# Kernel tuning notes

Hardware: AMD Instinct MI355X
Metric: run time of the kernel (lower is better)

The kernel has to match this reference:

```python
import jax, jax.numpy as jnp
import numpy as np

WD, WH, WW = 7, 7, 7  # 3D window size


def _relative_position_index():
    # Matches the torch buffer construction exactly.
    coords = np.stack(np.meshgrid(np.arange(WD), np.arange(WH), np.arange(WW), indexing='ij'))  # [3,wd,wh,ww]
    cf = coords.reshape(3, -1)                      # [3, n]
    rel = cf[:, :, None] - cf[:, None, :]           # [3, n, n]
    rel = rel.transpose(1, 2, 0).copy()             # [n, n, 3]
    rel[..., 0] += WD - 1
    rel[..., 1] += WH - 1
    rel[..., 2] += WW - 1
    rel[..., 0] *= (2 * WH - 1) * (2 * WW - 1)
    rel[..., 1] *= (2 * WW - 1)
    return rel.sum(-1).astype(np.int32)             # [n, n] in [0, 2197)


def setup_inputs() -> dict:
    key = jax.random.key(0)
    ks = jax.random.split(key, 10)
    DIM, H = 192, 6
    B, N, NW = 256, WD * WH * WW, 64  # b = batch*num_windows, NW divides B
    TABLE = (2 * WD - 1) * (2 * WH - 1) * (2 * WW - 1)  # 2197
    w_std = 0.02
    mask = jnp.where(jax.random.uniform(ks[2], (NW, N, N)) < 0.1, -100.0, 0.0).astype(jnp.float32)
    return {
        'x_q': jax.random.normal(ks[0], (B, N, DIM), jnp.float32),
        'x_kv': jax.random.normal(ks[1], (B, N, DIM), jnp.float32),
        'mask': mask,
        'q_w': jax.random.normal(ks[3], (DIM, DIM), jnp.float32) * w_std,
        'q_b': jnp.zeros((DIM,), jnp.float32),
        'kv_w': jax.random.normal(ks[4], (2 * DIM, DIM), jnp.float32) * w_std,
        'kv_b': jnp.zeros((2 * DIM,), jnp.float32),
        'proj_w': jax.random.normal(ks[5], (DIM, DIM), jnp.float32) * w_std,
        'proj_b': jnp.zeros((DIM,), jnp.float32),
        'rpb_table': jax.random.normal(ks[6], (TABLE, H), jnp.float32) * w_std,
        'rpi': jnp.asarray(_relative_position_index()),
    }


def reference(x_q, x_kv, mask, q_w, q_b, kv_w, kv_b, proj_w, proj_b, rpb_table, rpi):
    b, n, c = x_q.shape
    h = rpb_table.shape[-1]
    d = c // h
    scale = d ** (-0.5)
    # projections (torch Linear: y = x @ W.T + b)
    q = (x_q @ q_w.T + q_b).reshape(b, n, h, d)
    kv = x_kv @ kv_w.T + kv_b                      # [b, n, 2c]
    k = kv[..., :c].reshape(b, n, h, d)
    v = kv[..., c:].reshape(b, n, h, d)
    # windowed QK^T
    attn = jnp.einsum('bnhd,bmhd->bhnm', q * scale, k)  # [b, h, n, n]
    # gathered relative-position bias
    rpb = rpb_table[rpi[:n, :n].reshape(-1)].reshape(n, n, h).transpose(2, 0, 1)  # [h, n, n]
    attn = attn + rpb[None]
    # window mask add
    nw = mask.shape[0]
    attn = attn.reshape(b // nw, nw, h, n, n) + mask[None, :, None]
    attn = jax.nn.softmax(attn.reshape(b, h, n, n), axis=-1)
    out = jnp.einsum('bhnm,bmhd->bnhd', attn, v).reshape(b, n, c)
    return out @ proj_w.T + proj_b
```

## Files before the change

### kernel.cpp

```cpp
#include <hip/hip_runtime.h>
#include <hip/hip_bf16.h>
#include <cstdint>

#define B_    256
#define N_    343
#define C_    192
#define H_    6
#define D_    32
#define NW_   64
#define M_    (B_*N_)
#define NN_   (N_*N_)
#define VTS_  352
#define VLS_  360
#define RPG_  86
#define SCALE_ 0.17677669529663687f
#define LOG2E_ 1.4426950408889634f
#define SCALE_LOG2E_ (SCALE_ * LOG2E_)

typedef unsigned short ushort_t;
typedef __attribute__((ext_vector_type(8))) short short8;
typedef __attribute__((ext_vector_type(4))) float f32x4;
typedef __attribute__((ext_vector_type(16))) float f32x16;

__device__ __forceinline__ float b2f(unsigned int u) {
    return __uint_as_float(u << 16);
}
__device__ __forceinline__ unsigned int f2b(float f) {
    unsigned int x = __float_as_uint(f);
    x += 0x7FFFu + ((x >> 16) & 1u);
    return x >> 16;
}
__device__ __forceinline__ unsigned int cvt_pk(float a, float b) {
    unsigned int r;
    asm("v_cvt_pk_bf16_f32 %0, %1, %2" : "=v"(r) : "v"(a), "v"(b));
    return r;
}
__device__ __forceinline__ void pswap(unsigned int &x, unsigned int &y) {
    asm("v_permlane32_swap_b32 %0, %1" : "+v"(x), "+v"(y));
}

__global__ __launch_bounds__(256) void wcvt(
    const float* __restrict__ qw, const float* __restrict__ kvw,
    const float* __restrict__ pw, ushort_t* __restrict__ wb)
{
    int i = blockIdx.x * 256 + threadIdx.x;
    if (i >= 36864) return;
    float4 v;
    if (i < 9216)       v = ((const float4*)qw)[i];
    else if (i < 27648) v = ((const float4*)kvw)[i - 9216];
    else                v = ((const float4*)pw)[i - 27648];
    uint2 u;
    u.x = cvt_pk(v.x, v.y);
    u.y = cvt_pk(v.z, v.w);
    ((uint2*)wb)[i] = u;
}

__global__ __launch_bounds__(512, 2) void gemm_qkv(
    const float* __restrict__ xq, const float* __restrict__ xkv,
    const ushort_t* __restrict__ wb,
    const float* __restrict__ qbias, const float* __restrict__ kvbias,
    ushort_t* __restrict__ qx, ushort_t* __restrict__ kx,
    ushort_t* __restrict__ vtb)
{
    __shared__ ushort_t wls[192 * 200];
    __shared__ float    bls[192];

    const int t = threadIdx.x, wv = t >> 6, lane = t & 63;
    const int quad = lane >> 4, col = lane & 15;
    const int lbid = (blockIdx.x & 7) * 64 + (blockIdx.x >> 3);
    const int start = lbid * 2 + (lbid < 5 ? lbid : 5);
    const int cnt = 2 + (lbid < 5 ? 1 : 0);

    for (int ji = 0; ji < cnt; ++ji) {
        const int job = start + ji;
        const int mgrp = job / 3, jsel = job - mgrp * 3;
        const int m0 = mgrp * 256;
        const float* Xf = (jsel == 0) ? xq : xkv;
        const float* bias = (jsel == 0) ? qbias : (jsel == 1 ? kvbias : kvbias + 192);
        const float alpha = (jsel == 0) ? SCALE_LOG2E_ : 1.0f;

        if (ji) __syncthreads();
        {
            const ushort_t* W = wb + (size_t)jsel * 36864;
            for (int c = t; c < 4608; c += 512) {
                int row = c / 24, off = (c % 24) * 8;
                *(short8*)(wls + row * 200 + off) = *(const short8*)(W + row * 192 + off);
            }
            if (t < 48) ((float4*)bls)[t] = ((const float4*)bias)[t];
        }

        short8 xf[2][6];
        #pragma unroll
        for (int sub = 0; sub < 2; ++sub) {
            const float* xp = Xf + (size_t)(m0 + wv * 32 + sub * 16 + col) * 192;
            float4 a0[6], a1[6];
            #pragma unroll
            for (int kt = 0; kt < 6; ++kt) {
                a0[kt] = *(const float4*)(xp + kt * 32 + quad * 8);
                a1[kt] = *(const float4*)(xp + kt * 32 + quad * 8 + 4);
            }
            #pragma unroll
            for (int kt = 0; kt < 6; ++kt) {
                union { short8 s; unsigned int u[4]; } f;
                f.u[0] = cvt_pk(a0[kt].x, a0[kt].y);
                f.u[1] = cvt_pk(a0[kt].z, a0[kt].w);
                f.u[2] = cvt_pk(a1[kt].x, a1[kt].y);
                f.u[3] = cvt_pk(a1[kt].z, a1[kt].w);
                xf[sub][kt] = f.s;
            }
        }
        __syncthreads();

        f32x4 acc[2][12] = {};
        #pragma unroll
        for (int kt = 0; kt < 6; ++kt)
            #pragma unroll
            for (int ct = 0; ct < 12; ++ct) {
                short8 wf = *(const short8*)(wls + (ct * 16 + col) * 200 + kt * 32 + quad * 8);
                acc[0][ct] = __builtin_amdgcn_mfma_f32_16x16x32_bf16(wf, xf[0][kt], acc[0][ct], 0, 0, 0);
                acc[1][ct] = __builtin_amdgcn_mfma_f32_16x16x32_bf16(wf, xf[1][kt], acc[1][ct], 0, 0, 0);
            }

        if (jsel < 2) {
            ushort_t* o16 = (jsel == 0) ? qx : kx;
            #pragma unroll
            for (int sub = 0; sub < 2; ++sub) {
                int m = m0 + wv * 32 + sub * 16 + col;
                int bb = m / N_, nn = m - bb * N_;
                #pragma unroll
                for (int ct = 0; ct < 12; ++ct) {
                    float4 bv = *(const float4*)(bls + ct * 16 + quad * 4);
                    int hh = ct >> 1;
                    int dbase = (ct & 1) * 16 + quad * 4;
                    float v0 = (acc[sub][ct][0] + bv.x) * alpha;
                    float v1 = (acc[sub][ct][1] + bv.y) * alpha;
                    float v2 = (acc[sub][ct][2] + bv.z) * alpha;
                    float v3 = (acc[sub][ct][3] + bv.w) * alpha;
                    uint2 pk;
                    pk.x = cvt_pk(v0, v1);
                    pk.y = cvt_pk(v2, v3);
                    *(uint2*)(o16 + (((size_t)bb * H_ + hh) * N_ + nn) * D_ + dbase) = pk;
                }
            }
        } else {
            #pragma unroll
            for (int sub = 0; sub < 2; ++sub) {
                int m = m0 + wv * 32 + sub * 16 + col;
                int bb = m / N_, nn = m - bb * N_;
                #pragma unroll
                for (int ct = 0; ct < 12; ++ct) {
                    float4 bv = *(const float4*)(bls + ct * 16 + quad * 4);
                    int hh = ct >> 1;
                    int d0 = (ct & 1) * 16 + quad * 4;
                    unsigned int u01 = cvt_pk(acc[sub][ct][0] + bv.x, acc[sub][ct][1] + bv.y);
                    unsigned int u23 = cvt_pk(acc[sub][ct][2] + bv.z, acc[sub][ct][3] + bv.w);
                    ushort_t* vp = vtb + (((size_t)bb * H_ + hh) * D_ + d0) * VTS_ + nn;
                    vp[0]            = (ushort_t)u01;
                    vp[VTS_]         = (ushort_t)(u01 >> 16);
                    vp[2 * VTS_]     = (ushort_t)u23;
                    vp[3 * VTS_]     = (ushort_t)(u23 >> 16);
                }
            }
        }
    }
}

__global__ __launch_bounds__(512, 2) void gemm_out(
    const ushort_t* __restrict__ aob, const ushort_t* __restrict__ wb,
    const float* __restrict__ pbias, float* __restrict__ out)
{
    __shared__ ushort_t wls[192 * 200];

    const int t = threadIdx.x, wv = t >> 6, lane = t & 63;
    const int quad = lane >> 4, col = lane & 15;
    const int m0 = blockIdx.x * 256;
    const ushort_t* W = wb + (size_t)3 * 36864;

    short8 xf[2][6];
    #pragma unroll
    for (int sub = 0; sub < 2; ++sub) {
        const ushort_t* xp = aob + (size_t)(m0 + wv * 32 + sub * 16 + col) * 192;
        #pragma unroll
        for (int kt = 0; kt < 6; ++kt)
            xf[sub][kt] = *(const short8*)(xp + kt * 32 + quad * 8);
    }
    for (int c = t; c < 4608; c += 512) {
        int row = c / 24, off = (c % 24) * 8;
        *(short8*)(wls + row * 200 + off) = *(const short8*)(W + row * 192 + off);
    }
    __syncthreads();

    f32x4 acc[2][12] = {};
    #pragma unroll
    for (int kt = 0; kt < 6; ++kt)
        #pragma unroll
        for (int ct = 0; ct < 12; ++ct) {
            short8 wf = *(const short8*)(wls + (ct * 16 + col) * 200 + kt * 32 + quad * 8);
            acc[0][ct] = __builtin_amdgcn_mfma_f32_16x16x32_bf16(wf, xf[0][kt], acc[0][ct], 0, 0, 0);
            acc[1][ct] = __builtin_amdgcn_mfma_f32_16x16x32_bf16(wf, xf[1][kt], acc[1][ct], 0, 0, 0);
        }

    #pragma unroll
    for (int sub = 0; sub < 2; ++sub) {
        int m = m0 + wv * 32 + sub * 16 + col;
        #pragma unroll
        for (int ct = 0; ct < 12; ++ct) {
            float4 bv = *(const float4*)(pbias + ct * 16 + quad * 4);
            float4 vo;
            vo.x = acc[sub][ct][0] + bv.x; vo.y = acc[sub][ct][1] + bv.y;
            vo.z = acc[sub][ct][2] + bv.z; vo.w = acc[sub][ct][3] + bv.w;
            *(float4*)(out + (size_t)m * 192 + ct * 16 + quad * 4) = vo;
        }
    }
}

__global__ __launch_bounds__(256) void rpb_gather_b(
    const float* __restrict__ table, const int* __restrict__ rpi,
    ushort_t* __restrict__ rpbt)
{
    int n = blockIdx.x;
    for (int m = threadIdx.x; m < N_; m += 256) {
        int id = rpi[n * N_ + m];
        int mg = m >> 2, mi = m & 3;
        #pragma unroll
        for (int h = 0; h < H_; ++h)
            rpbt[((((size_t)h * RPG_ + mg) * N_) + n) * 4 + mi] =
                (ushort_t)f2b(table[(size_t)id * H_ + h] * LOG2E_);
    }
}

__global__ __launch_bounds__(256) void mask_bits(
    const float* __restrict__ mask, unsigned int* __restrict__ mbt)
{
    int gw   = blockIdx.x * 4 + (threadIdx.x >> 6);
    int lane = threadIdx.x & 63;
    int n = gw % N_, w = gw / N_;
    if (w >= NW_) return;
    const float* mrow = mask + ((size_t)w * N_ + n) * N_;
    #pragma unroll
    for (int seg = 0; seg < 6; ++seg) {
        int m = seg * 64 + lane;
        float v = (m < N_) ? mrow[m] : -100.f;
        unsigned long long bm = __ballot(v > -50.f);
        if (lane < 2)
            mbt[((size_t)w * 12 + seg * 2 + lane) * N_ + n] =
                (unsigned int)(bm >> (lane * 32));
    }
}

__global__ __launch_bounds__(256) void vt_pad(ushort_t* __restrict__ vtb)
{
    int bh = blockIdx.x;
    for (int i = threadIdx.x; i < D_ * (VTS_ - N_); i += 256) {
        int d = i / (VTS_ - N_), m = N_ + i % (VTS_ - N_);
        vtb[((size_t)bh * D_ + d) * VTS_ + m] = 0;
    }
}

__global__ __launch_bounds__(256, 3) void attn_mfma(
    const ushort_t* __restrict__ qb, const ushort_t* __restrict__ kb,
    const ushort_t* __restrict__ vtb, const ushort_t* __restrict__ rpbt,
    const unsigned int* __restrict__ mbt, ushort_t* __restrict__ aob)
{
    __shared__ ushort_t ks[352 * 40];
    __shared__ ushort_t vls[32 * VLS_];

    const int t = threadIdx.x, wv = t >> 6, lane = t & 63;
    const int hh = lane >> 5, c = lane & 31;
    const int lid = blockIdx.x;
    const int wg = (lid & 7) * 576 + (lid >> 3);
    const int qt = wg % 3;
    const int bhx = wg / 3;
    const int h = bhx % H_, b = bhx / H_;
    const int bh = b * H_ + h;
    const int w  = b & (NW_ - 1);
    const int n0 = qt * 128 + wv * 32;

    const ushort_t* kbase = kb + (size_t)bh * (N_ * D_);
    for (int cc = t; cc < (N_ * D_) / 8; cc += 256) {
        int row = cc >> 2, off = (cc & 3) * 8;
        *(short8*)(ks + row * 40 + off) = *(const short8*)(kbase + cc * 8);
    }
    for (int cc = t; cc < 360; cc += 256) ks[13720 + cc] = 0;

    {
        const int vd = t >> 3, vj0 = t & 7;
        const ushort_t* vsrc = vtb + (size_t)bh * (D_ * VTS_) + (size_t)vd * VTS_;
        ushort_t* vdst = vls + vd * VLS_;
        #pragma unroll
        for (int j = 0; j < 6; ++j) {
            int jj = vj0 + j * 8;
            if (jj < 44)
                *(short8*)(vdst + jj * 8) = *(const short8*)(vsrc + jj * 8);
        }
    }

    int nn = n0 + c; if (nn > N_ - 1) nn = N_ - 1;
    const ushort_t* qp = qb + ((size_t)bh * N_ + nn) * D_;
    short8 qf0 = *(const short8*)(qp + hh * 8);
    short8 qf1 = *(const short8*)(qp + 16 + hh * 8);

    unsigned int dwv[12];
    {
        const unsigned int* mbp = mbt + (size_t)w * 12 * N_ + nn;
        #pragma unroll
        for (int i = 0; i < 12; ++i) dwv[i] = mbp[i * N_];
    }
    const uint2* rp2h = (const uint2*)rpbt + (size_t)h * (RPG_ * N_) + nn
                        + (size_t)hh * N_;

    __syncthreads();

    f32x16 oacc = {};
    float sum = 0.f;

    #pragma unroll
    for (int kt = 0; kt < 11; ++kt) {
        const ushort_t* krow = ks + (kt * 32 + c) * 40 + hh * 8;
        short8 ka  = *(const short8*)(krow);
        short8 kb2 = *(const short8*)(krow + 16);
        unsigned int nibs = dwv[kt] >> (hh * 4);
        f32x16 s;
        #pragma unroll
        for (int g = 0; g < 4; ++g) {
            if (kt == 10 && g == 3) {
                s[12] = -3.0e38f; s[13] = -3.0e38f;
                s[14] = -3.0e38f; s[15] = -3.0e38f;
            } else {
                uint2 rv = rp2h[(kt * 8 + 2 * g) * (size_t)N_];
                unsigned int nib = (nibs >> (g * 8)) & 0xFu;
                s[4*g+0] = (nib & 1u) ? b2f(rv.x & 0xffffu) : -3.0e38f;
                s[4*g+1] = (nib & 2u) ? b2f(rv.x >> 16)     : -3.0e38f;
                s[4*g+2] = (nib & 4u) ? b2f(rv.y & 0xffffu) : -3.0e38f;
                s[4*g+3] = (nib & 8u) ? b2f(rv.y >> 16)     : -3.0e38f;
            }
        }
        s = __builtin_amdgcn_mfma_f32_32x32x16_bf16(ka,  qf0, s, 0, 0, 0);
        s = __builtin_amdgcn_mfma_f32_32x32x16_bf16(kb2, qf1, s, 0, 0, 0);

        unsigned int pk[8];
        #pragma unroll
        for (int g = 0; g < 4; ++g) {
            float e0 = __builtin_exp2f(s[4*g+0]);
            float e1 = __builtin_exp2f(s[4*g+1]);
            float e2 = __builtin_exp2f(s[4*g+2]);
            float e3 = __builtin_exp2f(s[4*g+3]);
            sum += (e0 + e1) + (e2 + e3);
            pk[2*g]   = cvt_pk(e0, e1);
            pk[2*g+1] = cvt_pk(e2, e3);
        }
        pswap(pk[0], pk[2]);
        pswap(pk[1], pk[3]);
        pswap(pk[4], pk[6]);
        pswap(pk[5], pk[7]);
        union { short8 s8; unsigned int u[4]; } pf1, pf2;
        pf1.u[0] = pk[0]; pf1.u[1] = pk[1]; pf1.u[2] = pk[2]; pf1.u[3] = pk[3];
        pf2.u[0] = pk[4]; pf2.u[1] = pk[5]; pf2.u[2] = pk[6]; pf2.u[3] = pk[7];

        const ushort_t* vrow = vls + c * VLS_ + kt * 32 + hh * 8;
        short8 vf1 = *(const short8*)(vrow);
        short8 vf2 = *(const short8*)(vrow + 16);
        oacc = __builtin_amdgcn_mfma_f32_32x32x16_bf16(vf1, pf1.s8, oacc, 0, 0, 0);
        oacc = __builtin_amdgcn_mfma_f32_32x32x16_bf16(vf2, pf2.s8, oacc, 0, 0, 0);
    }

    sum += __shfl_xor(sum, 32);

    int n = n0 + c;
    if (n < N_) {
        float inv = 1.0f / sum;
        ushort_t* op = aob + ((size_t)b * N_ + n) * C_ + h * D_ + hh * 4;
        #pragma unroll
        for (int g = 0; g < 4; ++g) {
            uint2 pkk;
            pkk.x = cvt_pk(oacc[4*g+0] * inv, oacc[4*g+1] * inv);
            pkk.y = cvt_pk(oacc[4*g+2] * inv, oacc[4*g+3] * inv);
            *(uint2*)(op + g * 8) = pkk;
        }
    }
}

extern "C" void kernel_launch(void* const* d_in, const int* in_sizes, int n_in,
                              void* d_out, int out_size, void* d_ws, size_t ws_size,
                              hipStream_t stream)
{
    const float* x_q    = (const float*)d_in[0];
    const float* x_kv   = (const float*)d_in[1];
    const float* mask   = (const float*)d_in[2];
    const float* q_w    = (const float*)d_in[3];
    const float* q_b    = (const float*)d_in[4];
    const float* kv_w   = (const float*)d_in[5];
    const float* kv_b   = (const float*)d_in[6];
    const float* proj_w = (const float*)d_in[7];
    const float* proj_b = (const float*)d_in[8];
    const float* rpb_t  = (const float*)d_in[9];
    const int*   rpi    = (const int*)d_in[10];
    float* out = (float*)d_out;

    const size_t QKV  = (size_t)B_ * H_ * N_ * D_;
    const size_t QKV2 = (size_t)B_ * H_ * D_ * VTS_;
    char* ws = (char*)d_ws;
    ushort_t* qx   = (ushort_t*)ws;
    ushort_t* kx   = qx + QKV;
    ushort_t* vtb  = kx + QKV;
    ushort_t* aob  = vtb + QKV2;
    ushort_t* rpbt = aob + QKV;
    ushort_t* wb   = rpbt + (size_t)H_ * RPG_ * N_ * 4;
    unsigned int* mbt = (unsigned int*)(wb + 147456);

    wcvt<<<144, 256, 0, stream>>>(q_w, kv_w, proj_w, wb);
    rpb_gather_b<<<N_, 256, 0, stream>>>(rpb_t, rpi, rpbt);
    mask_bits<<<(NW_ * N_) / 4, 256, 0, stream>>>(mask, mbt);
    vt_pad<<<B_ * H_, 256, 0, stream>>>(vtb);
    gemm_qkv<<<512, 512, 0, stream>>>(
        x_q, x_kv, wb, q_b, kv_b, qx, kx, vtb);
    attn_mfma<<<4608, 256, 0, stream>>>(qx, kx, vtb, rpbt, mbt, aob);
    gemm_out<<<343, 512, 0, stream>>>(aob, wb, proj_b, out);
}
```

Before: 389.7 us.

## Use atomic work queue in QKV GEMM and read K directly from global in attention

The QKV projection kernel drops its static job partition and pulls jobs from a global atomic counter, which wcvt resets. The counter lives at the start of the attention-output buffer, which is only written later. The attention kernel stops staging K in shared memory and loads K fragments straight from global memory. It also raises the occupancy hint from 3 to 7 blocks per CU, trading shared-memory reuse of K for more resident waves. The risks are extra global/L2 traffic for K and register pressure under the tighter launch bound.

```diff
diff --git a/kernel.cpp b/kernel.cpp
--- a/kernel.cpp
+++ b/kernel.cpp
@@ -13,6 +13,7 @@
 #define VTS_  352
 #define VLS_  360
 #define RPG_  86
+#define NJOB_ 1029
 #define SCALE_ 0.17677669529663687f
 #define LOG2E_ 1.4426950408889634f
 #define SCALE_LOG2E_ (SCALE_ * LOG2E_)
@@ -41,9 +42,11 @@
 
 __global__ __launch_bounds__(256) void wcvt(
     const float* __restrict__ qw, const float* __restrict__ kvw,
-    const float* __restrict__ pw, ushort_t* __restrict__ wb)
+    const float* __restrict__ pw, ushort_t* __restrict__ wb,
+    unsigned int* __restrict__ ctr)
 {
     int i = blockIdx.x * 256 + threadIdx.x;
+    if (i == 0) *ctr = 0;
     if (i >= 36864) return;
     float4 v;
     if (i < 9216)       v = ((const float4*)qw)[i];
@@ -60,26 +63,28 @@
     const ushort_t* __restrict__ wb,
     const float* __restrict__ qbias, const float* __restrict__ kvbias,
     ushort_t* __restrict__ qx, ushort_t* __restrict__ kx,
-    ushort_t* __restrict__ vtb)
+    ushort_t* __restrict__ vtb, unsigned int* __restrict__ ctr)
 {
     __shared__ ushort_t wls[192 * 200];
     __shared__ float    bls[192];
+    __shared__ int      sjob;
 
     const int t = threadIdx.x, wv = t >> 6, lane = t & 63;
     const int quad = lane >> 4, col = lane & 15;
-    const int lbid = (blockIdx.x & 7) * 64 + (blockIdx.x >> 3);
-    const int start = lbid * 2 + (lbid < 5 ? lbid : 5);
-    const int cnt = 2 + (lbid < 5 ? 1 : 0);
-
-    for (int ji = 0; ji < cnt; ++ji) {
-        const int job = start + ji;
+
+    for (;;) {
+        __syncthreads();
+        if (t == 0) sjob = (int)atomicAdd(ctr, 1u);
+        __syncthreads();
+        const int job = sjob;
+        if (job >= NJOB_) break;
+
         const int mgrp = job / 3, jsel = job - mgrp * 3;
         const int m0 = mgrp * 256;
         const float* Xf = (jsel == 0) ? xq : xkv;
         const float* bias = (jsel == 0) ? qbias : (jsel == 1 ? kvbias : kvbias + 192);
         const float alpha = (jsel == 0) ? SCALE_LOG2E_ : 1.0f;
 
-        if (ji) __syncthreads();
         {
             const ushort_t* W = wb + (size_t)jsel * 36864;
             for (int c = t; c < 4608; c += 512) {
@@ -257,12 +262,11 @@
     }
 }
 
-__global__ __launch_bounds__(256, 3) void attn_mfma(
+__global__ __launch_bounds__(256, 7) void attn_mfma(
     const ushort_t* __restrict__ qb, const ushort_t* __restrict__ kb,
     const ushort_t* __restrict__ vtb, const ushort_t* __restrict__ rpbt,
     const unsigned int* __restrict__ mbt, ushort_t* __restrict__ aob)
 {
-    __shared__ ushort_t ks[352 * 40];
     __shared__ ushort_t vls[32 * VLS_];
 
     const int t = threadIdx.x, wv = t >> 6, lane = t & 63;
@@ -276,13 +280,6 @@
     const int w  = b & (NW_ - 1);
     const int n0 = qt * 128 + wv * 32;
 
-    const ushort_t* kbase = kb + (size_t)bh * (N_ * D_);
-    for (int cc = t; cc < (N_ * D_) / 8; cc += 256) {
-        int row = cc >> 2, off = (cc & 3) * 8;
-        *(short8*)(ks + row * 40 + off) = *(const short8*)(kbase + cc * 8);
-    }
-    for (int cc = t; cc < 360; cc += 256) ks[13720 + cc] = 0;
-
     {
         const int vd = t >> 3, vj0 = t & 7;
         const ushort_t* vsrc = vtb + (size_t)bh * (D_ * VTS_) + (size_t)vd * VTS_;
@@ -308,6 +305,7 @@
     }
     const uint2* rp2h = (const uint2*)rpbt + (size_t)h * (RPG_ * N_) + nn
                         + (size_t)hh * N_;
+    const ushort_t* kB = kb + (size_t)bh * (N_ * D_) + (size_t)c * D_ + hh * 8;
 
     __syncthreads();
 
@@ -316,7 +314,7 @@
 
     #pragma unroll
     for (int kt = 0; kt < 11; ++kt) {
-        const ushort_t* krow = ks + (kt * 32 + c) * 40 + hh * 8;
+        const ushort_t* krow = kB + kt * 32 * D_;
         short8 ka  = *(const short8*)(krow);
         short8 kb2 = *(const short8*)(krow + 16);
         unsigned int nibs = dwv[kt] >> (hh * 4);
@@ -407,13 +405,14 @@
     ushort_t* rpbt = aob + QKV;
     ushort_t* wb   = rpbt + (size_t)H_ * RPG_ * N_ * 4;
     unsigned int* mbt = (unsigned int*)(wb + 147456);
-
-    wcvt<<<144, 256, 0, stream>>>(q_w, kv_w, proj_w, wb);
+    unsigned int* ctr = (unsigned int*)aob;
+
+    wcvt<<<144, 256, 0, stream>>>(q_w, kv_w, proj_w, wb, ctr);
     rpb_gather_b<<<N_, 256, 0, stream>>>(rpb_t, rpi, rpbt);
     mask_bits<<<(NW_ * N_) / 4, 256, 0, stream>>>(mask, mbt);
     vt_pad<<<B_ * H_, 256, 0, stream>>>(vtb);
     gemm_qkv<<<512, 512, 0, stream>>>(
-        x_q, x_kv, wb, q_b, kv_b, qx, kx, vtb);
+        x_q, x_kv, wb, q_b, kv_b, qx, kx, vtb, ctr);
     attn_mfma<<<4608, 256, 0, stream>>>(qx, kx, vtb, rpbt, mbt, aob);
     gemm_out<<<343, 512, 0, stream>>>(aob, wb, proj_b, out);
 }
```

New measurement: 371.8 us. 1.05x faster.
